# Kernel tuning notes

Measured on AMD Instinct MI355X. Metric: run time of the kernel, lower is better.

Reference implementation:

```python
import jax, jax.numpy as jnp
import numpy as np

CUTOFF = 5.0
RBF_DIM = 32
M0, M1, M2 = 128, 64, 32          # node multiplicities for l=0,1,2
DIM_NODE = M0 + 3 * M1 + 5 * M2   # 480
MSG = 64                          # message multiplicity per l
NBLK = 3
MAX_Z = 100


def _sph_harm(d):
    # component-normalized real spherical harmonics up to lmax=2; d: [E,3] unit vectors
    x, y, z = d[:, 0], d[:, 1], d[:, 2]
    s3, s5, s15 = jnp.sqrt(3.0), jnp.sqrt(5.0), jnp.sqrt(15.0)
    return jnp.stack([
        jnp.ones_like(x),
        s3 * x, s3 * y, s3 * z,
        s15 * x * y, s15 * y * z, 0.5 * s5 * (3.0 * z * z - 1.0),
        s15 * x * z, 0.5 * s15 * (x * x - y * y),
    ], axis=-1)  # [E, 9]


def _rbf(d):
    centers = jnp.linspace(0.0, CUTOFF, RBF_DIM)
    width = CUTOFF / (RBF_DIM - 1)
    return jnp.exp(-0.5 * ((d[:, None] - centers) / width) ** 2)  # [E, RBF_DIM]


def _irrep_norm(x):
    # per-node RMS norm of each irrep block (l=0,1,2)
    eps = 1e-6
    parts = []
    for off, mul, dim in ((0, M0, 1), (M0, M1, 3), (M0 + 3 * M1, M2, 5)):
        blk = x[:, off:off + mul * dim].reshape(-1, mul, dim)
        rms = jnp.sqrt(jnp.mean(jnp.sum(blk * blk, axis=-1), axis=-1, keepdims=True) + eps)
        parts.append((blk / rms[..., None]).reshape(-1, mul * dim))
    return jnp.concatenate(parts, axis=-1)


def setup_inputs() -> dict:
    key = jax.random.key(0)
    ks = jax.random.split(key, 20)
    B, N, E = 32, 128, 131072
    BN = B * N

    z = jax.random.randint(ks[0], (B, N), 1, MAX_Z + 1)
    mask = jnp.ones((B, N), jnp.float32)
    edge_src = jax.random.randint(ks[1], (E,), 0, BN)
    edge_dst = jax.random.randint(ks[2], (E,), 0, BN)
    edge_weight = jax.random.uniform(ks[3], (E,), minval=0.1, maxval=CUTOFF)
    ed = jax.random.normal(ks[4], (E, 3), jnp.float32)
    ed = ed / jnp.linalg.norm(ed, axis=-1, keepdims=True)
    edge_vec = ed * edge_weight[:, None]

    def nrm(k, shape, fan_in):
        return jax.random.normal(k, shape, jnp.float32) / np.sqrt(fan_in)

    params = {
        "z_emb": jax.random.normal(ks[5], (MAX_Z + 1, M0), jnp.float32),
        "W_in": nrm(ks[6], (M0, M0), M0),
        "Wp": nrm(ks[7], (NBLK, M0, 3 * MSG), M0),
        "rW1": nrm(ks[8], (NBLK, RBF_DIM, 64), RBF_DIM),
        "rb1": jnp.zeros((NBLK, 64), jnp.float32),
        "rW2": nrm(ks[9], (NBLK, 64, 3 * MSG), 64),
        "rb2": jnp.zeros((NBLK, 3 * MSG), jnp.float32),
        "Wo0": nrm(ks[10], (NBLK, MSG, M0), MSG),
        "Wo1": nrm(ks[11], (NBLK, MSG, M1), MSG),
        "Wo2": nrm(ks[12], (NBLK, MSG, M2), MSG),
        "res_scale": jnp.full((NBLK,), 1.0, jnp.float32),
    }
    return {"z": z, "mask": mask, "edge_src": edge_src, "edge_dst": edge_dst,
            "edge_weight": edge_weight, "edge_vec": edge_vec, **params}


def reference(z, mask, edge_src, edge_dst, edge_weight, edge_vec,
              z_emb, W_in, Wp, rW1, rb1, rW2, rb2, Wo0, Wo1, Wo2, res_scale):
    B, N = z.shape
    BN = B * N
    fmask = mask.reshape(BN)

    # element embedding -> o3.Linear(0e -> irreps_node): only scalar channels are produced
    zf = z_emb[z.reshape(BN)]                                    # [BN, node_attr]
    x0 = zf @ W_in                                               # [BN, M0]
    x = jnp.concatenate([x0, jnp.zeros((BN, DIM_NODE - M0), x0.dtype)], axis=-1)
    x = x * fmask[:, None]

    elen = edge_weight
    edir = edge_vec / jnp.clip(elen, 1e-8)[:, None]
    rbf = _rbf(jnp.minimum(elen, CUTOFF))                        # [E, RBF_DIM]
    sh = _sph_harm(edir)                                         # [E, 9]
    fcut = 0.5 * (jnp.cos(jnp.pi * jnp.minimum(elen / CUTOFF, 1.0)) + 1.0)

    for b in range(NBLK):
        s = x[:, :M0]
        proj = s[edge_src] @ Wp[b]                               # [E, 3*MSG] gather + GEMM
        h = jax.nn.silu(rbf @ rW1[b] + rb1[b])
        r = h @ rW2[b] + rb2[b]                                  # [E, 3*MSG] radial weights
        w = proj * r * fcut[:, None]
        w0, w1, w2 = w[:, :MSG], w[:, MSG:2 * MSG], w[:, 2 * MSG:]
        msg0 = w0 * sh[:, 0:1]                                   # [E, MSG]
        msg1 = w1[:, :, None] * sh[:, None, 1:4]                 # [E, MSG, 3]
        msg2 = w2[:, :, None] * sh[:, None, 4:9]                 # [E, MSG, 5]
        m0 = jax.ops.segment_sum(msg0, edge_dst, num_segments=BN)
        m1 = jax.ops.segment_sum(msg1, edge_dst, num_segments=BN)
        m2 = jax.ops.segment_sum(msg2, edge_dst, num_segments=BN)
        u0 = m0 @ Wo0[b]                                         # [BN, M0]
        u1 = jnp.einsum('ncd,ck->nkd', m1, Wo1[b]).reshape(BN, 3 * M1)
        u2 = jnp.einsum('ncd,ck->nkd', m2, Wo2[b]).reshape(BN, 5 * M2)
        x = x + res_scale[b] * jnp.concatenate([u0, u1, u2], axis=-1)

    x = _irrep_norm(x) * fmask[:, None]
    return x.reshape(B, N, DIM_NODE)
```

## Files before the change

### kernel.cpp

```cpp
#include <hip/hip_runtime.h>
#include <math.h>

#define M0 128
#define M1 64
#define M2 32
#define DIMN 480
#define MSGC 64
#define NBLK 3
#define RBFD 32
#define NT 512
#define TCHUNK 32
#define NNP 16
#define GNPB 4
#define PSTR 68
#define WROWS 224
#define FCUT 5.0f

typedef unsigned int   u32;
typedef unsigned short u16;

__device__ __forceinline__ u16 f2bf(float f) {
    u32 u = __float_as_uint(f);
    u32 r = (u + 0x7fffu + ((u >> 16) & 1u)) >> 16;
    return (u16)r;
}
__device__ __forceinline__ float bf_lo(u32 v) { return __uint_as_float(v << 16); }
__device__ __forceinline__ float bf_hi(u32 v) { return __uint_as_float(v & 0xffff0000u); }

struct __align__(16) ERec {
    int   src;
    int   ti;
    float fr;
    float fc;
    float sh[8];
};

__global__ void k_zero(int* __restrict__ p, int n) {
    int i = blockIdx.x * blockDim.x + threadIdx.x;
    if (i < n) p[i] = 0;
}

__global__ void k_count(const int* __restrict__ dst, int* __restrict__ counts, int E) {
    int e = blockIdx.x * blockDim.x + threadIdx.x;
    if (e >= E) return;
    atomicAdd(&counts[dst[e]], 1);
}

__global__ __launch_bounds__(1024) void k_scan(const int* __restrict__ counts,
                                               int* __restrict__ offs,
                                               int* __restrict__ cursor, int n) {
    __shared__ int ws[1024];
    int t = threadIdx.x;
    int4 v = ((const int4*)counts)[t];
    int s0 = v.x, s1 = s0 + v.y, s2 = s1 + v.z, s3 = s2 + v.w;
    ws[t] = s3;
    __syncthreads();
    for (int d = 1; d < 1024; d <<= 1) {
        int val = (t >= d) ? ws[t - d] : 0;
        __syncthreads();
        ws[t] += val;
        __syncthreads();
    }
    int excl = (t == 0) ? 0 : ws[t - 1];
    int4 o;
    o.x = excl; o.y = excl + s0; o.z = excl + s1; o.w = excl + s2;
    ((int4*)offs)[t] = o;
    ((int4*)cursor)[t] = o;
    if (t == 1023) offs[n] = excl + s3;
}

__global__ void k_build(const float* __restrict__ ew, const float* __restrict__ ev,
                        const int* __restrict__ src, const int* __restrict__ dst,
                        int* __restrict__ cursor, ERec* __restrict__ rec, int E) {
    int e = blockIdx.x * blockDim.x + threadIdx.x;
    if (e >= E) return;
    float len = ew[e];
    float inv = 1.0f / fmaxf(len, 1e-8f);
    float x = ev[e * 3 + 0] * inv;
    float y = ev[e * 3 + 1] * inv;
    float z = ev[e * 3 + 2] * inv;
    const float s3 = 1.7320508075688772f, s5 = 2.23606797749979f, s15 = 3.872983346207417f;
    ERec r;
    r.src = src[e];
    float u = fminf(len, FCUT) * ((float)(NT - 1) / FCUT);
    int ti = (int)u;
    ti = min(ti, NT - 2);
    r.ti = ti;
    r.fr = u - (float)ti;
    float t = fminf(len / FCUT, 1.0f);
    float fc = 0.5f * (cosf(3.14159265358979323846f * t) + 1.0f);
    r.fc = fc;
    r.sh[0] = s3 * x * fc;
    r.sh[1] = s3 * y * fc;
    r.sh[2] = s3 * z * fc;
    r.sh[3] = s15 * x * y * fc;
    r.sh[4] = s15 * y * z * fc;
    r.sh[5] = 0.5f * s5 * (3.0f * z * z - 1.0f) * fc;
    r.sh[6] = s15 * x * z * fc;
    r.sh[7] = 0.5f * s15 * (x * x - y * y) * fc;
    int p = atomicAdd(&cursor[dst[e]], 1);
    rec[p] = r;
}

#define RTB (NBLK * (NT / TCHUNK))
__global__ __launch_bounds__(256) void k_rtab(const float* __restrict__ rW1,
                                              const float* __restrict__ rb1,
                                              const float* __restrict__ rW2,
                                              const float* __restrict__ rb2,
                                              u32* __restrict__ rPI,
                                              const float* __restrict__ Wo0,
                                              const float* __restrict__ Wo1,
                                              const float* __restrict__ Wo2,
                                              float* __restrict__ WoT) {
    int blk = blockIdx.x;
    int tid = threadIdx.x;
    if (blk >= RTB) {
        int idx = (blk - RTB) * 256 + tid;
        const int wtot = NBLK * WROWS * 64;
        if (idx >= wtot) return;
        int b = idx / (WROWS * 64);
        int rem = idx - b * (WROWS * 64);
        int row = rem >> 6, c = rem & 63;
        float v;
        if (row < 128)      v = Wo0[(size_t)b * MSGC * M0 + c * M0 + row];
        else if (row < 192) v = Wo1[(size_t)b * MSGC * M1 + c * M1 + (row - 128)];
        else                v = Wo2[(size_t)b * MSGC * M2 + c * M2 + (row - 192)];
        WoT[idx] = v;
        return;
    }
    int b = blk / (NT / TCHUNK);
    int t0 = (blk % (NT / TCHUNK)) * TCHUNK;
    __shared__ float rbf_s[TCHUNK + 1][RBFD];
    __shared__ float hh_s[64][TCHUNK + 1];

    const float wdt = FCUT / (float)(RBFD - 1);
    for (int idx = tid; idx < (TCHUNK + 1) * RBFD; idx += 256) {
        int tt = idx >> 5, k = idx & 31;
        int te = min(t0 + tt, NT - 1);
        float len = (float)te * (FCUT / (float)(NT - 1));
        float d0 = (len - (float)k * wdt) / wdt;
        rbf_s[tt][k] = expf(-0.5f * d0 * d0);
    }
    __syncthreads();
    const float* W1 = rW1 + b * RBFD * 64;
    for (int idx = tid; idx < (TCHUNK + 1) * 64; idx += 256) {
        int tt = idx / 64, jj = idx & 63;
        float a = rb1[b * 64 + jj];
        #pragma unroll 8
        for (int k = 0; k < RBFD; ++k) a += rbf_s[tt][k] * W1[k * 64 + jj];
        hh_s[jj][tt] = a / (1.0f + expf(-a));
    }
    __syncthreads();
    if (tid < 192) {
        int c = tid;
        const float* W2 = rW2 + b * 64 * 192;
        float w2r[64];
        #pragma unroll
        for (int k = 0; k < 64; ++k) w2r[k] = W2[k * 192 + c];
        float b2 = rb2[b * 192 + c];
        int lane = c & 63, q = c >> 6;
        u32* out = rPI + ((size_t)b * NT * 64) * 4;
        float prev = 0.0f;
        for (int tt = 0; tt <= TCHUNK; ++tt) {
            float acc = b2;
            #pragma unroll
            for (int k = 0; k < 64; ++k) acc += hh_s[k][tt] * w2r[k];
            if (tt > 0) {
                int t = t0 + tt - 1;
                out[((size_t)t * 64 + lane) * 4 + q] =
                    (u32)f2bf(prev) | ((u32)f2bf(acc) << 16);
            }
            prev = acc;
        }
    }
}

__global__ __launch_bounds__(192) void k_proj0(const int* __restrict__ z,
                                               const float* __restrict__ mask,
                                               const float* __restrict__ zemb,
                                               const float* __restrict__ Win,
                                               const float* __restrict__ Wp,
                                               float* __restrict__ x,
                                               u16* __restrict__ PI) {
    int n0 = blockIdx.x * NNP;
    int j = threadIdx.x;
    __shared__ float zf[NNP][M0];
    __shared__ float xs[NNP][M0];
    for (int idx = j; idx < NNP * M0; idx += 192) {
        int n = idx >> 7, c = idx & 127;
        zf[n][c] = zemb[z[n0 + n] * M0 + c];
    }
    __syncthreads();
    for (int idx = j; idx < NNP * M0; idx += 192) {
        int n = idx >> 7, c = idx & 127;
        float acc = 0.0f;
        for (int k = 0; k < M0; ++k) acc += zf[n][k] * Win[k * M0 + c];
        acc *= mask[n0 + n];
        xs[n][c] = acc;
        x[(size_t)(n0 + n) * DIMN + c] = acc;
    }
    for (int idx = j; idx < NNP * (DIMN - M0); idx += 192) {
        int n = idx / (DIMN - M0), c = idx - n * (DIMN - M0);
        x[(size_t)(n0 + n) * DIMN + M0 + c] = 0.0f;
    }
    __syncthreads();
    float acc[NNP];
    #pragma unroll
    for (int u = 0; u < NNP; ++u) acc[u] = 0.0f;
    for (int k = 0; k < M0; ++k) {
        float wv = Wp[k * 192 + j];
        #pragma unroll
        for (int u = 0; u < NNP; ++u) acc[u] += xs[u][k] * wv;
    }
    int lane = j & 63, q = j >> 6;
    #pragma unroll
    for (int u = 0; u < NNP; ++u)
        PI[((size_t)(n0 + u) * 64 + lane) * 4 + q] = f2bf(acc[u]);
}

__global__ __launch_bounds__(192) void k_proj(const float* __restrict__ x,
                                              const float* __restrict__ Wp,
                                              u16* __restrict__ PI) {
    int n0 = blockIdx.x * NNP;
    int j = threadIdx.x;
    __shared__ float xs[NNP][M0];
    for (int idx = j; idx < NNP * M0; idx += 192) {
        int n = idx >> 7, c = idx & 127;
        xs[n][c] = x[(size_t)(n0 + n) * DIMN + c];
    }
    __syncthreads();
    float acc[NNP];
    #pragma unroll
    for (int u = 0; u < NNP; ++u) acc[u] = 0.0f;
    for (int k = 0; k < M0; ++k) {
        float wv = Wp[k * 192 + j];
        #pragma unroll
        for (int u = 0; u < NNP; ++u) acc[u] += xs[u][k] * wv;
    }
    int lane = j & 63, q = j >> 6;
    #pragma unroll
    for (int u = 0; u < NNP; ++u)
        PI[((size_t)(n0 + u) * 64 + lane) * 4 + q] = f2bf(acc[u]);
}

__global__ __launch_bounds__(512) void k_gather(const u16* __restrict__ PI,
                                                const u32* __restrict__ rPI,
                                                const ERec* __restrict__ rec,
                                                const int* __restrict__ offs,
                                                const float* __restrict__ WoT,
                                                const float* __restrict__ res_scale, int b,
                                                float* __restrict__ x,
                                                const float* __restrict__ mask,
                                                float* __restrict__ out) {
    int t = threadIdx.x;
    int w = t >> 6;
    int j = t & 63;
    int local = w >> 1;
    int par = w & 1;
    int n0 = blockIdx.x * GNPB;
    int n = n0 + local;
    int e0 = offs[n], e1 = offs[n + 1];

    float m0 = 0.0f;
    float m1a[3] = {0, 0, 0};
    float m2a[5] = {0, 0, 0, 0, 0};

    __shared__ float mbuf[8][9 * PSTR];
    __shared__ float invs[GNPB][3];

    {
        int i0 = e0 + par;
        if (i0 < e1) {
            const int last = e1 - 1;
            int nIter = (e1 - i0 + 1) >> 1;
            float4 A0, A1, A2, B0, B1, B2, C0, C1, C2;
            {
                int ia = __builtin_amdgcn_readfirstlane(i0);
                const float4* p = (const float4*)(rec + ia);
                A0 = p[0]; A1 = p[1]; A2 = p[2];
            }
            {
                int v = i0 + 2; v = v < e1 ? v : last;
                int ib = __builtin_amdgcn_readfirstlane(v);
                const float4* p = (const float4*)(rec + ib);
                B0 = p[0]; B1 = p[1]; B2 = p[2];
            }
            {
                int v = i0 + 4; v = v < e1 ? v : last;
                int ic = __builtin_amdgcn_readfirstlane(v);
                const float4* p = (const float4*)(rec + ic);
                C0 = p[0]; C1 = p[1]; C2 = p[2];
            }
            uint4 rA, rB, rC; uint2 pA, pB, pC;
            {
                int s = __float_as_int(A0.x), ti = __float_as_int(A0.y);
                rA = ((const uint4*)(rPI + ((size_t)ti << 8)))[j];
                pA = ((const uint2*)(PI + ((size_t)s << 8)))[j];
            }
            {
                int s = __float_as_int(B0.x), ti = __float_as_int(B0.y);
                rB = ((const uint4*)(rPI + ((size_t)ti << 8)))[j];
                pB = ((const uint2*)(PI + ((size_t)s << 8)))[j];
            }
            #pragma unroll 4
            for (int k = 0; k < nIter; ++k) {
                int i = i0 + (k << 1);
                float4 D0, D1, D2;
                {
                    int v = i + 6; v = v < e1 ? v : last;
                    int id = __builtin_amdgcn_readfirstlane(v);
                    const float4* p = (const float4*)(rec + id);
                    D0 = p[0]; D1 = p[1]; D2 = p[2];
                }
                {
                    int s = __float_as_int(C0.x), ti = __float_as_int(C0.y);
                    rC = ((const uint4*)(rPI + ((size_t)ti << 8)))[j];
                    pC = ((const uint2*)(PI + ((size_t)s << 8)))[j];
                }
                float fr = A0.z, fc = A0.w;
                float la = bf_lo(rA.x);
                float va = la + fr * (bf_hi(rA.x) - la);
                float p0 = __uint_as_float(pA.x << 16);
                float p1 = __uint_as_float(pA.x & 0xffff0000u);
                float p2 = __uint_as_float(pA.y << 16);
                m0 = fmaf(p0 * va, fc, m0);
                float lb = bf_lo(rA.y);
                float vb = lb + fr * (bf_hi(rA.y) - lb);
                float w1 = p1 * vb;
                m1a[0] += w1 * A1.x;
                m1a[1] += w1 * A1.y;
                m1a[2] += w1 * A1.z;
                float lc = bf_lo(rA.z);
                float vc = lc + fr * (bf_hi(rA.z) - lc);
                float w2 = p2 * vc;
                m2a[0] += w2 * A1.w;
                m2a[1] += w2 * A2.x;
                m2a[2] += w2 * A2.y;
                m2a[3] += w2 * A2.z;
                m2a[4] += w2 * A2.w;
                A0 = B0; A1 = B1; A2 = B2;
                B0 = C0; B1 = C1; B2 = C2;
                C0 = D0; C1 = D1; C2 = D2;
                rA = rB; pA = pB; rB = rC; pB = pC;
            }
        }
    }

    mbuf[w][0 * PSTR + j] = m0;
    #pragma unroll
    for (int d = 0; d < 3; ++d) mbuf[w][(1 + d) * PSTR + j] = m1a[d];
    #pragma unroll
    for (int d = 0; d < 5; ++d) mbuf[w][(4 + d) * PSTR + j] = m2a[d];
    __syncthreads();
    #pragma unroll
    for (int u = 0; u < GNPB; ++u)
        for (int c = t; c < 9 * PSTR; c += 512)
            mbuf[2 * u][c] += mbuf[2 * u + 1][c];
    __syncthreads();

    float rs = res_scale[b];
    int o = t;
    if (o < DIMN) {
        int row, mbase;
        if (o < M0) {
            row = o; mbase = 0;
        } else if (o < M0 + 3 * M1) {
            int q = o - M0, k = q / 3, d = q - 3 * k;
            row = 128 + k; mbase = (1 + d) * PSTR;
        } else {
            int q = o - (M0 + 3 * M1), k = q / 5, d = q - 5 * k;
            row = 192 + k; mbase = (4 + d) * PSTR;
        }
        const float4* Wv = (const float4*)(WoT + (size_t)row * 64);
        float a0 = 0, a1 = 0, a2 = 0, a3 = 0;
        #pragma unroll
        for (int c4 = 0; c4 < 16; ++c4) {
            float4 wv = Wv[c4];
            float4 v0 = *(const float4*)&mbuf[0][mbase + 4 * c4];
            float4 v1 = *(const float4*)&mbuf[2][mbase + 4 * c4];
            float4 v2 = *(const float4*)&mbuf[4][mbase + 4 * c4];
            float4 v3 = *(const float4*)&mbuf[6][mbase + 4 * c4];
            a0 += wv.x * v0.x + wv.y * v0.y + wv.z * v0.z + wv.w * v0.w;
            a1 += wv.x * v1.x + wv.y * v1.y + wv.z * v1.z + wv.w * v1.w;
            a2 += wv.x * v2.x + wv.y * v2.y + wv.z * v2.z + wv.w * v2.w;
            a3 += wv.x * v3.x + wv.y * v3.y + wv.z * v3.z + wv.w * v3.w;
        }
        if (b < NBLK - 1) {
            x[(size_t)(n0 + 0) * DIMN + o] += rs * a0;
            x[(size_t)(n0 + 1) * DIMN + o] += rs * a1;
            x[(size_t)(n0 + 2) * DIMN + o] += rs * a2;
            x[(size_t)(n0 + 3) * DIMN + o] += rs * a3;
        } else {
            mbuf[1][o] = x[(size_t)(n0 + 0) * DIMN + o] + rs * a0;
            mbuf[3][o] = x[(size_t)(n0 + 1) * DIMN + o] + rs * a1;
            mbuf[5][o] = x[(size_t)(n0 + 2) * DIMN + o] + rs * a2;
            mbuf[7][o] = x[(size_t)(n0 + 3) * DIMN + o] + rs * a3;
        }
    }

    if (b < NBLK - 1) return;

    __syncthreads();
    if (w < GNPB) {
        const float* xf = mbuf[2 * w + 1];
        float s0 = 0, s1 = 0, s2 = 0;
        for (int c = j; c < DIMN; c += 64) {
            float v = xf[c];
            if (c < 128) s0 += v * v;
            else if (c < 320) s1 += v * v;
            else s2 += v * v;
        }
        #pragma unroll
        for (int d = 32; d > 0; d >>= 1) {
            s0 += __shfl_down(s0, d);
            s1 += __shfl_down(s1, d);
            s2 += __shfl_down(s2, d);
        }
        if (j == 0) {
            invs[w][0] = rsqrtf(s0 / (float)M0 + 1e-6f);
            invs[w][1] = rsqrtf(s1 / (float)M1 + 1e-6f);
            invs[w][2] = rsqrtf(s2 / (float)M2 + 1e-6f);
        }
    }
    __syncthreads();
    if (o < DIMN) {
        int cls = (o < 128) ? 0 : (o < 320) ? 1 : 2;
        #pragma unroll
        for (int u = 0; u < GNPB; ++u) {
            float fm = mask[n0 + u];
            out[(size_t)(n0 + u) * DIMN + o] = mbuf[2 * u + 1][o] * invs[u][cls] * fm;
        }
    }
}

extern "C" void kernel_launch(void* const* d_in, const int* in_sizes, int n_in,
                              void* d_out, int out_size, void* d_ws, size_t ws_size,
                              hipStream_t stream) {
    const int*   z    = (const int*)d_in[0];
    const float* mask = (const float*)d_in[1];
    const int*   esrc = (const int*)d_in[2];
    const int*   edst = (const int*)d_in[3];
    const float* ew   = (const float*)d_in[4];
    const float* ev   = (const float*)d_in[5];
    const float* zemb = (const float*)d_in[6];
    const float* Win  = (const float*)d_in[7];
    const float* Wp   = (const float*)d_in[8];
    const float* rW1  = (const float*)d_in[9];
    const float* rb1  = (const float*)d_in[10];
    const float* rW2  = (const float*)d_in[11];
    const float* rb2  = (const float*)d_in[12];
    const float* Wo0  = (const float*)d_in[13];
    const float* Wo1  = (const float*)d_in[14];
    const float* Wo2  = (const float*)d_in[15];
    const float* res  = (const float*)d_in[16];

    const int BN = in_sizes[0];
    const int E  = in_sizes[2];

    char* w = (char*)d_ws;
    float* x    = (float*)w;  w += (size_t)BN * DIMN * 4;
    u16*   PI   = (u16*)w;    w += (size_t)BN * 256 * 2;
    u32*   rPI  = (u32*)w;    w += (size_t)NBLK * NT * 256 * 4;
    ERec*  rec  = (ERec*)w;   w += (size_t)E * sizeof(ERec);
    float* WoT  = (float*)w;  w += (size_t)NBLK * WROWS * 64 * 4;
    int* counts = (int*)w;   w += (size_t)BN * 4;
    int* offs   = (int*)w;   w += (size_t)(BN + 4) * 4;
    int* cursor = (int*)w;   w += (size_t)BN * 4;

    k_zero<<<(BN + 255) / 256, 256, 0, stream>>>(counts, BN);
    k_count<<<(E + 255) / 256, 256, 0, stream>>>(edst, counts, E);
    k_scan<<<1, 1024, 0, stream>>>(counts, offs, cursor, BN);
    k_build<<<(E + 255) / 256, 256, 0, stream>>>(ew, ev, esrc, edst, cursor, rec, E);
    {
        int wotb = (NBLK * WROWS * 64 + 255) / 256;
        k_rtab<<<RTB + wotb, 256, 0, stream>>>(rW1, rb1, rW2, rb2, rPI,
                                               Wo0, Wo1, Wo2, WoT);
    }
    k_proj0<<<BN / NNP, 192, 0, stream>>>(z, mask, zemb, Win, Wp, x, PI);

    for (int b = 0; b < NBLK; ++b) {
        if (b > 0)
            k_proj<<<BN / NNP, 192, 0, stream>>>(x, Wp + (size_t)b * M0 * 192, PI);
        k_gather<<<BN / GNPB, 512, 0, stream>>>(PI, rPI + (size_t)b * NT * 256, rec, offs,
                                                WoT + (size_t)b * WROWS * 64,
                                                res, b, x, mask, (float*)d_out);
    }
}
```

Baseline: 216.9 us.

## Fuse next-block projection into gather kernel epilogue with double-buffered PI

Removes the separate k_proj launch between blocks: the gather kernel now computes the updated scalar features in shared memory and immediately projects them through the next block's Wp, writing into a ping-pong PI buffer. This avoids re-reading x from global memory and two extra launches, but the projection now runs with 4 nodes per block, so Wp is reread more often and cannot be amortized over 16 nodes. k_proj0 is also shrunk to 4 nodes per block, which gives more blocks.

```diff
diff --git a/kernel.cpp b/kernel.cpp
--- a/kernel.cpp
+++ b/kernel.cpp
@@ -10,7 +10,7 @@
 #define RBFD 32
 #define NT 512
 #define TCHUNK 32
-#define NNP 16
+#define NNP0 4
 #define GNPB 4
 #define PSTR 68
 #define WROWS 224
@@ -182,16 +182,16 @@
                                                const float* __restrict__ Wp,
                                                float* __restrict__ x,
                                                u16* __restrict__ PI) {
-    int n0 = blockIdx.x * NNP;
+    int n0 = blockIdx.x * NNP0;
     int j = threadIdx.x;
-    __shared__ float zf[NNP][M0];
-    __shared__ float xs[NNP][M0];
-    for (int idx = j; idx < NNP * M0; idx += 192) {
+    __shared__ float zf[NNP0][M0];
+    __shared__ float xs[NNP0][M0];
+    for (int idx = j; idx < NNP0 * M0; idx += 192) {
         int n = idx >> 7, c = idx & 127;
         zf[n][c] = zemb[z[n0 + n] * M0 + c];
     }
     __syncthreads();
-    for (int idx = j; idx < NNP * M0; idx += 192) {
+    for (int idx = j; idx < NNP0 * M0; idx += 192) {
         int n = idx >> 7, c = idx & 127;
         float acc = 0.0f;
         for (int k = 0; k < M0; ++k) acc += zf[n][k] * Win[k * M0 + c];
@@ -199,55 +199,32 @@
         xs[n][c] = acc;
         x[(size_t)(n0 + n) * DIMN + c] = acc;
     }
-    for (int idx = j; idx < NNP * (DIMN - M0); idx += 192) {
+    for (int idx = j; idx < NNP0 * (DIMN - M0); idx += 192) {
         int n = idx / (DIMN - M0), c = idx - n * (DIMN - M0);
         x[(size_t)(n0 + n) * DIMN + M0 + c] = 0.0f;
     }
     __syncthreads();
-    float acc[NNP];
+    float acc[NNP0];
     #pragma unroll
-    for (int u = 0; u < NNP; ++u) acc[u] = 0.0f;
+    for (int u = 0; u < NNP0; ++u) acc[u] = 0.0f;
     for (int k = 0; k < M0; ++k) {
         float wv = Wp[k * 192 + j];
         #pragma unroll
-        for (int u = 0; u < NNP; ++u) acc[u] += xs[u][k] * wv;
+        for (int u = 0; u < NNP0; ++u) acc[u] += xs[u][k] * wv;
     }
     int lane = j & 63, q = j >> 6;
     #pragma unroll
-    for (int u = 0; u < NNP; ++u)
+    for (int u = 0; u < NNP0; ++u)
         PI[((size_t)(n0 + u) * 64 + lane) * 4 + q] = f2bf(acc[u]);
 }
 
-__global__ __launch_bounds__(192) void k_proj(const float* __restrict__ x,
-                                              const float* __restrict__ Wp,
-                                              u16* __restrict__ PI) {
-    int n0 = blockIdx.x * NNP;
-    int j = threadIdx.x;
-    __shared__ float xs[NNP][M0];
-    for (int idx = j; idx < NNP * M0; idx += 192) {
-        int n = idx >> 7, c = idx & 127;
-        xs[n][c] = x[(size_t)(n0 + n) * DIMN + c];
-    }
-    __syncthreads();
-    float acc[NNP];
-    #pragma unroll
-    for (int u = 0; u < NNP; ++u) acc[u] = 0.0f;
-    for (int k = 0; k < M0; ++k) {
-        float wv = Wp[k * 192 + j];
-        #pragma unroll
-        for (int u = 0; u < NNP; ++u) acc[u] += xs[u][k] * wv;
-    }
-    int lane = j & 63, q = j >> 6;
-    #pragma unroll
-    for (int u = 0; u < NNP; ++u)
-        PI[((size_t)(n0 + u) * 64 + lane) * 4 + q] = f2bf(acc[u]);
-}
-
-__global__ __launch_bounds__(512) void k_gather(const u16* __restrict__ PI,
+__global__ __launch_bounds__(512) void k_gather(const u16* __restrict__ PIin,
+                                                u16* __restrict__ PIout,
                                                 const u32* __restrict__ rPI,
                                                 const ERec* __restrict__ rec,
                                                 const int* __restrict__ offs,
                                                 const float* __restrict__ WoT,
+                                                const float* __restrict__ WpNext,
                                                 const float* __restrict__ res_scale, int b,
                                                 float* __restrict__ x,
                                                 const float* __restrict__ mask,
@@ -295,12 +272,12 @@
             {
                 int s = __float_as_int(A0.x), ti = __float_as_int(A0.y);
                 rA = ((const uint4*)(rPI + ((size_t)ti << 8)))[j];
-                pA = ((const uint2*)(PI + ((size_t)s << 8)))[j];
+                pA = ((const uint2*)(PIin + ((size_t)s << 8)))[j];
             }
             {
                 int s = __float_as_int(B0.x), ti = __float_as_int(B0.y);
                 rB = ((const uint4*)(rPI + ((size_t)ti << 8)))[j];
-                pB = ((const uint2*)(PI + ((size_t)s << 8)))[j];
+                pB = ((const uint2*)(PIin + ((size_t)s << 8)))[j];
             }
             #pragma unroll 4
             for (int k = 0; k < nIter; ++k) {
@@ -315,7 +292,7 @@
                 {
                     int s = __float_as_int(C0.x), ti = __float_as_int(C0.y);
                     rC = ((const uint4*)(rPI + ((size_t)ti << 8)))[j];
-                    pC = ((const uint2*)(PI + ((size_t)s << 8)))[j];
+                    pC = ((const uint2*)(PIin + ((size_t)s << 8)))[j];
                 }
                 float fr = A0.z, fc = A0.w;
                 float la = bf_lo(rA.x);
@@ -385,20 +362,35 @@
             a2 += wv.x * v2.x + wv.y * v2.y + wv.z * v2.z + wv.w * v2.w;
             a3 += wv.x * v3.x + wv.y * v3.y + wv.z * v3.z + wv.w * v3.w;
         }
+        a0 = x[(size_t)(n0 + 0) * DIMN + o] + rs * a0;
+        a1 = x[(size_t)(n0 + 1) * DIMN + o] + rs * a1;
+        a2 = x[(size_t)(n0 + 2) * DIMN + o] + rs * a2;
+        a3 = x[(size_t)(n0 + 3) * DIMN + o] + rs * a3;
         if (b < NBLK - 1) {
-            x[(size_t)(n0 + 0) * DIMN + o] += rs * a0;
-            x[(size_t)(n0 + 1) * DIMN + o] += rs * a1;
-            x[(size_t)(n0 + 2) * DIMN + o] += rs * a2;
-            x[(size_t)(n0 + 3) * DIMN + o] += rs * a3;
+            x[(size_t)(n0 + 0) * DIMN + o] = a0;
+            x[(size_t)(n0 + 1) * DIMN + o] = a1;
+            x[(size_t)(n0 + 2) * DIMN + o] = a2;
+            x[(size_t)(n0 + 3) * DIMN + o] = a3;
+            if (o < M0) {
+                mbuf[1][o] = a0; mbuf[3][o] = a1; mbuf[5][o] = a2; mbuf[7][o] = a3;
+            }
         } else {
-            mbuf[1][o] = x[(size_t)(n0 + 0) * DIMN + o] + rs * a0;
-            mbuf[3][o] = x[(size_t)(n0 + 1) * DIMN + o] + rs * a1;
-            mbuf[5][o] = x[(size_t)(n0 + 2) * DIMN + o] + rs * a2;
-            mbuf[7][o] = x[(size_t)(n0 + 3) * DIMN + o] + rs * a3;
-        }
-    }
-
-    if (b < NBLK - 1) return;
+            mbuf[1][o] = a0; mbuf[3][o] = a1; mbuf[5][o] = a2; mbuf[7][o] = a3;
+        }
+    }
+
+    if (b < NBLK - 1) {
+        __syncthreads();
+        for (int oo = t; oo < GNPB * 192; oo += 512) {
+            int u = oo / 192, c = oo - u * 192;
+            const float* xf = mbuf[2 * u + 1];
+            float acc = 0.0f;
+            #pragma unroll 8
+            for (int k = 0; k < M0; ++k) acc += xf[k] * WpNext[k * 192 + c];
+            PIout[((size_t)(n0 + u) * 64 + (c & 63)) * 4 + (c >> 6)] = f2bf(acc);
+        }
+        return;
+    }
 
     __syncthreads();
     if (w < GNPB) {
@@ -459,7 +451,8 @@
 
     char* w = (char*)d_ws;
     float* x    = (float*)w;  w += (size_t)BN * DIMN * 4;
-    u16*   PI   = (u16*)w;    w += (size_t)BN * 256 * 2;
+    u16*   PIa  = (u16*)w;    w += (size_t)BN * 256 * 2;
+    u16*   PIb  = (u16*)w;    w += (size_t)BN * 256 * 2;
     u32*   rPI  = (u32*)w;    w += (size_t)NBLK * NT * 256 * 4;
     ERec*  rec  = (ERec*)w;   w += (size_t)E * sizeof(ERec);
     float* WoT  = (float*)w;  w += (size_t)NBLK * WROWS * 64 * 4;
@@ -476,13 +469,15 @@
         k_rtab<<<RTB + wotb, 256, 0, stream>>>(rW1, rb1, rW2, rb2, rPI,
                                                Wo0, Wo1, Wo2, WoT);
     }
-    k_proj0<<<BN / NNP, 192, 0, stream>>>(z, mask, zemb, Win, Wp, x, PI);
-
+    k_proj0<<<BN / NNP0, 192, 0, stream>>>(z, mask, zemb, Win, Wp, x, PIa);
+
+    u16* pibuf[2] = {PIa, PIb};
     for (int b = 0; b < NBLK; ++b) {
-        if (b > 0)
-            k_proj<<<BN / NNP, 192, 0, stream>>>(x, Wp + (size_t)b * M0 * 192, PI);
-        k_gather<<<BN / GNPB, 512, 0, stream>>>(PI, rPI + (size_t)b * NT * 256, rec, offs,
+        const float* WpNext = Wp + (size_t)(b + 1 < NBLK ? b + 1 : 0) * M0 * 192;
+        k_gather<<<BN / GNPB, 512, 0, stream>>>(pibuf[b & 1], pibuf[(b + 1) & 1],
+                                                rPI + (size_t)b * NT * 256,
+                                                rec, offs,
                                                 WoT + (size_t)b * WROWS * 64,
-                                                res, b, x, mask, (float*)d_out);
-    }
-}
+                                                WpNext, res, b, x, mask, (float*)d_out);
+    }
+}
```

Result: faster. 201.7 us (-7.0%).
